# Performance work log

Hardware: AMD Instinct MI355X
Metric: run time of the kernel (lower is better)

## Reference

```python
import jax, jax.numpy as jnp
import numpy as np

T, B = 384, 128
IN_DIM, HID, OUT_DIM = 512, 1024, 512


def _lstm_step(h, c, x_t, Wx, Wh, b):
    # x_t: [B, D], h/c: [B, H]; gates order: i, f, g, o
    gates = x_t @ Wx + h @ Wh + b  # [B, 4H]
    i, f, g, o = jnp.split(gates, 4, axis=-1)
    c_new = jax.nn.sigmoid(f) * c + jax.nn.sigmoid(i) * jnp.tanh(g)
    h_new = jax.nn.sigmoid(o) * jnp.tanh(c_new)
    return h_new, c_new


def setup_inputs() -> dict:
    key = jax.random.key(0)
    ks = jax.random.split(key, 9)
    s_in = 1.0 / np.sqrt(IN_DIM)
    s_h = 1.0 / np.sqrt(HID)
    s_o = 1.0 / np.sqrt(OUT_DIM)
    return {
        "x": jax.random.normal(ks[0], (T, B, IN_DIM), dtype=jnp.float32),
        "hidden_state": jnp.zeros((1, B, HID), dtype=jnp.float32),
        "cell_state": jnp.zeros((1, B, HID), dtype=jnp.float32),
        "enc_Wx": jax.random.normal(ks[1], (IN_DIM, 4 * HID), dtype=jnp.float32) * s_in,
        "enc_Wh": jax.random.normal(ks[2], (HID, 4 * HID), dtype=jnp.float32) * s_h,
        "enc_b": jnp.zeros((4 * HID,), dtype=jnp.float32),
        "dec_Wx": jax.random.normal(ks[3], (OUT_DIM, 4 * HID), dtype=jnp.float32) * s_o,
        "dec_Wh": jax.random.normal(ks[4], (HID, 4 * HID), dtype=jnp.float32) * s_h,
        "dec_b": jnp.zeros((4 * HID,), dtype=jnp.float32),
        "fc_W": jax.random.normal(ks[5], (HID, OUT_DIM), dtype=jnp.float32) * s_h,
        "fc_b": jnp.zeros((OUT_DIM,), dtype=jnp.float32),
    }


def reference(x, hidden_state, cell_state, enc_Wx, enc_Wh, enc_b,
              dec_Wx, dec_Wh, dec_b, fc_W, fc_b):
    # ---- encoder: run LSTM over T steps, keep only final hidden state ----
    h0, c0 = hidden_state[0], cell_state[0]  # [B, H]

    def enc_step(carry, x_t):
        h, c = carry
        h, c = _lstm_step(h, c, x_t, enc_Wx, enc_Wh, enc_b)
        return (h, c), None

    (h_enc, _), _ = jax.lax.scan(enc_step, (h0, c0), x)

    y0 = jnp.zeros((B, OUT_DIM), dtype=x.dtype)
    c_dec0 = jnp.zeros((B, HID), dtype=x.dtype)

    def dec_step(carry, _):
        y, h, c = carry
        h, c = _lstm_step(h, c, y, dec_Wx, dec_Wh, dec_b)
        y = jax.nn.softmax(h @ fc_W + fc_b, axis=-1)  # softmax over dim=2
        return (y, h, c), y

    _, output = jax.lax.scan(dec_step, (y0, h_enc, c_dec0), None, length=T)
    return output  # [T, B, OUT_DIM]
```

## Files before the change

kernel.cpp:

```cpp
#include <hip/hip_runtime.h>


#define TS 384

typedef __attribute__((ext_vector_type(8))) short bf16x8;
typedef __attribute__((ext_vector_type(4))) float f32x4;

#define WS_XR 4096u
#define XR_SLOT 262144u
#define WS_HP (WS_XR + 4u*XR_SLOT)
#define HP_BUF 524288u
#define WS_FPN (WS_HP + 2u*HP_BUF)
#define WS_TOTAL (WS_FPN + 2097152u)

#define MFMA __builtin_amdgcn_mfma_f32_16x16x32_bf16

__device__ __forceinline__ unsigned short bf16r(float v) {
  unsigned u = __float_as_uint(v);
  u += 0x7FFFu + ((u >> 16) & 1u);
  return (unsigned short)(u >> 16);
}
__device__ __forceinline__ float bf2f(unsigned short h) {
  return __uint_as_float(((unsigned)h) << 16);
}
__device__ __forceinline__ void split2(float v, short& hi, short& lo) {
  unsigned short h = bf16r(v);
  float r = v - bf2f(h);
  hi = (short)h; lo = (short)bf16r(r);
}
__device__ __forceinline__ float sigm(float v)  { return 1.0f / (1.0f + __expf(-v)); }
__device__ __forceinline__ float tanhfa(float v){ return 1.0f - 2.0f / (__expf(2.0f*v) + 1.0f); }

__device__ __forceinline__ void st_u64(void* p, unsigned long long v) {
  __hip_atomic_store((unsigned long long*)p, v, __ATOMIC_RELAXED, __HIP_MEMORY_SCOPE_AGENT);
}
__device__ __forceinline__ unsigned long long ld_u64(const void* p) {
  return __hip_atomic_load((const unsigned long long*)p, __ATOMIC_RELAXED, __HIP_MEMORY_SCOPE_AGENT);
}
__device__ __forceinline__ void st_u32(unsigned* p, unsigned v) {
  __hip_atomic_store(p, v, __ATOMIC_RELAXED, __HIP_MEMORY_SCOPE_AGENT);
}
__device__ __forceinline__ void st_f32(float* p, float v) {
  __hip_atomic_store(p, v, __ATOMIC_RELAXED, __HIP_MEMORY_SCOPE_AGENT);
}
__device__ __forceinline__ float ld_f32(const float* p) {
  return __hip_atomic_load(p, __ATOMIC_RELAXED, __HIP_MEMORY_SCOPE_AGENT);
}
union FRAG { unsigned long long q[2]; bf16x8 v; };
__device__ __forceinline__ bf16x8 ld_frag(const short* base) {
  FRAG u;
  u.q[0] = ld_u64(base);
  u.q[1] = ld_u64(base + 4);
  return u.v;
}

__device__ __forceinline__ void setflag(unsigned* flag, unsigned val) {
  asm volatile("s_waitcnt vmcnt(0)" ::: "memory");
  __syncthreads();
  if (threadIdx.x == 0)
    __hip_atomic_store(flag, val, __ATOMIC_RELAXED, __HIP_MEMORY_SCOPE_AGENT);
}
__device__ __forceinline__ void wait_hier(const unsigned* flags, unsigned* pub,
    int aggIdx, int nPub, unsigned target, bool fence, int* sDead) {
  const int t = threadIdx.x;
  if (aggIdx >= 0) {
    if (t < 8) {
      const unsigned long long* q = (const unsigned long long*)(flags + aggIdx * 32 + t * 4);
      unsigned spins = 0;
      for (;;) {
        unsigned long long q0 = ld_u64(q), q1 = ld_u64(q + 1);
        bool ok = ((unsigned)q0 >= target) && ((unsigned)(q0 >> 32) >= target)
               && ((unsigned)q1 >= target) && ((unsigned)(q1 >> 32) >= target);
        if (__all(ok)) break;
        __builtin_amdgcn_s_sleep(1);
        if (++spins > (1u << 19)) { if (t == 0) *sDead = 1; break; }
      }
    }
    if (t == 0) st_u32(&pub[aggIdx], target);
  }
  if (t == 0) {
    unsigned spins = 0;
    for (;;) {
      bool ok = true;
      #pragma unroll
      for (int i = 0; i < 4; ++i) {
        if (i * 2 < nPub) {
          unsigned long long q0 = ld_u64((const unsigned long long*)pub + i);
          if (!((unsigned)q0 >= target && (unsigned)(q0 >> 32) >= target)) ok = false;
        }
      }
      if (ok) break;
      __builtin_amdgcn_s_sleep(1);
      if (++spins > (1u << 19)) { *sDead = 1; break; }
    }
    if (fence) __builtin_amdgcn_fence(__ATOMIC_ACQUIRE, "agent");
  }
  __syncthreads();
}
__device__ __forceinline__ void wait64(const unsigned* flags, unsigned target, int* sDead) {
  if (threadIdx.x < 16) {
    const unsigned long long* q = (const unsigned long long*)(flags + threadIdx.x * 4);
    unsigned spins = 0;
    for (;;) {
      unsigned long long q0 = ld_u64(q), q1 = ld_u64(q + 1);
      bool ok = ((unsigned)q0 >= target) && ((unsigned)(q0 >> 32) >= target)
             && ((unsigned)q1 >= target) && ((unsigned)(q1 >> 32) >= target);
      if (__all(ok)) break;
      __builtin_amdgcn_s_sleep(1);
      if (++spins > (1u << 19)) { if (threadIdx.x == 0) *sDead = 1; break; }
    }
  }
  __syncthreads();
}

__device__ void load_gate_weights(const float* __restrict__ Wx, const float* __restrict__ Wh,
                                  int p, short* sBh, short* sBl) {
  for (int idx = threadIdx.x; idx < 24576; idx += 1024) {
    int j = idx & 7, l = (idx >> 3) & 63, kb = idx >> 9;
    int k = kb * 32 + ((l >> 4) << 3) + j;
    int c = l & 15;
    int gcol = (c >> 2) * 1024 + p * 4 + (c & 3);
    float wv = (k < 512) ? Wx[(size_t)k * 4096 + gcol]
                         : Wh[(size_t)(k - 512) * 4096 + gcol];
    short hi, lo; split2(wv, hi, lo);
    sBh[idx] = hi; sBl[idx] = lo;
  }
}
__device__ void load_fc_weights(const float* __restrict__ fcW, int kg, int cg,
                                short* sFh, short* sFl) {
  for (int idx = threadIdx.x; idx < 4096; idx += 1024) {
    int j = idx & 7, l = (idx >> 3) & 63, kb = idx >> 9;
    int unit = kg * 256 + kb * 32 + ((l >> 4) << 3) + j;
    int col = cg * 16 + (l & 15);
    short hi, lo; split2(fcW[(size_t)unit * 512 + col], hi, lo);
    sFh[idx] = hi; sFl[idx] = lo;
  }
}

template<int NKB, int D>
__device__ __forceinline__ void gg_pipe(const short* AH_, const short* AL_,
    const short* BH_, const short* BL_, int mt, int l,
    int kbA0, int kbB0, f32x4* acc)
{
  const bf16x8* AH = (const bf16x8*)AH_;
  const bf16x8* AL = (const bf16x8*)AL_;
  const bf16x8* BH = (const bf16x8*)BH_;
  const bf16x8* BL = (const bf16x8*)BL_;
  bf16x8 pah[D], pal[D];
  #pragma unroll
  for (int i = 0; i < D; ++i) {
    pah[i] = AH[((kbA0 + i) * 8 + mt) * 64 + l];
    pal[i] = AL[((kbA0 + i) * 8 + mt) * 64 + l];
  }
  #pragma unroll
  for (int i = 0; i < NKB; ++i) {
    bf16x8 ah = pah[i % D], al = pal[i % D];
    if (i + D < NKB) {
      pah[i % D] = AH[((kbA0 + i + D) * 8 + mt) * 64 + l];
      pal[i % D] = AL[((kbA0 + i + D) * 8 + mt) * 64 + l];
    }
    bf16x8 bh = BH[(kbB0 + i) * 64 + l];
    bf16x8 bl = BL[(kbB0 + i) * 64 + l];
    const int a = (i & 1) * 3;
    acc[a + 0] = MFMA(ah, bh, acc[a + 0], 0, 0, 0);
    acc[a + 1] = MFMA(ah, bl, acc[a + 1], 0, 0, 0);
    acc[a + 2] = MFMA(al, bh, acc[a + 2], 0, 0, 0);
  }
}
__device__ __forceinline__ void gg_finish(f32x4* acc, int kh, int mt, int l,
                                          float* LDSgate) {
  f32x4 s = (acc[0] + acc[3]) + ((acc[1] + acc[4]) + (acc[2] + acc[5]));
  const int col = l & 15, r0 = mt * 16 + ((l >> 4) << 2);
  float* plane = LDSgate + kh * 2176;
  #pragma unroll
  for (int j = 0; j < 4; ++j) plane[(r0 + j) * 17 + col] = s[j];
}

__device__ __forceinline__ void conv_x(const float* __restrict__ xsrc,
                                       short* dstH, short* dstL, int p, int tl) {
  if (tl < 32) {
    int g = p * 32 + tl;
    int l = g & 63, mt = (g >> 6) & 7, kb = g >> 9;
    int row = mt * 16 + (l & 15), k = kb * 32 + ((l >> 4) << 3);
    const float* xs = xsrc + (size_t)row * 512 + k;
    unsigned long long h64[2] = {0, 0}, l64[2] = {0, 0};
    #pragma unroll
    for (int j = 0; j < 8; ++j) {
      short hi, lo; split2(xs[j], hi, lo);
      h64[j >> 2] |= (unsigned long long)(unsigned short)hi << ((j & 3) * 16);
      l64[j >> 2] |= (unsigned long long)(unsigned short)lo << ((j & 3) * 16);
    }
    int off = g * 8;
    st_u64(dstH + off, h64[0]); st_u64(dstH + off + 4, h64[1]);
    st_u64(dstL + off, l64[0]); st_u64(dstL + off + 4, l64[1]);
  }
}

__global__ void __launch_bounds__(1024, 1)
lstm9(const float* __restrict__ x, const float* __restrict__ h0p,
      const float* __restrict__ c0p, const float* __restrict__ eWx,
      const float* __restrict__ eWh, const float* __restrict__ eb,
      const float* __restrict__ dWx, const float* __restrict__ dWh,
      const float* __restrict__ db, const float* __restrict__ fcW,
      const float* __restrict__ fcb, float* __restrict__ out,
      char* __restrict__ ws)
{
  __shared__ __align__(16) short sBh[24576], sBl[24576];
  __shared__ __align__(16) short sFh[4096], sFl[4096];
  __shared__ float LDSgate[2 * 2176];
  __shared__ unsigned hsplit[512];
  __shared__ float ybuf[512];
  __shared__ float red[16];
  __shared__ int sDead;

  const int p = blockIdx.x, t = threadIdx.x;
  const int w = t >> 6, l = t & 63;
  const int mt = w & 7, kh = w >> 3;
  if (t == 0) sDead = 0;

  unsigned* hflag = (unsigned*)ws;
  unsigned* yflag = (unsigned*)(ws + 1024);
  unsigned* fflag = (unsigned*)(ws + 2048);
  unsigned* hpub  = (unsigned*)(ws + 3072);
  unsigned* ypub  = (unsigned*)(ws + 3200);
  unsigned* fpub  = (unsigned*)(ws + 3328);

  const int hagg = (p < 8) ? p : -1;
  const int yagg = (p >= 8 && p < 12) ? p - 8 : -1;
  const int fagg = (p >= 12 && p < 16) ? p - 12 : -1;

  short* xrH[4]; short* xrL[4];
  #pragma unroll
  for (int s4 = 0; s4 < 4; ++s4) {
    xrH[s4] = (short*)(ws + WS_XR + s4 * XR_SLOT);
    xrL[s4] = (short*)(ws + WS_XR + s4 * XR_SLOT + 131072u);
  }
  short* hpH[2]; short* hpL[2];
  #pragma unroll
  for (int b2 = 0; b2 < 2; ++b2) {
    hpH[b2] = (short*)(ws + WS_HP + b2 * HP_BUF);
    hpL[b2] = (short*)(ws + WS_HP + b2 * HP_BUF + 262144u);
  }
  float* fp = (float*)(ws + WS_FPN);

  const int row_pw = t & 127, u_pw = (t >> 7) & 3;

  load_gate_weights(eWx, eWh, p, sBh, sBl);
  conv_x(x, xrH[0], xrL[0], p, t);
  conv_x(x + 65536, xrH[1], xrL[1], p, t);
  if (t < 64) {
    int hg = p * 64 + t;
    int ll = hg & 63, mtt = (hg >> 6) & 7, hk = hg >> 9;
    int row = mtt * 16 + (ll & 15), k = hk * 32 + ((ll >> 4) << 3);
    const float* hs = h0p + (size_t)row * 1024 + k;
    unsigned long long h64[2] = {0, 0}, l64[2] = {0, 0};
    #pragma unroll
    for (int j = 0; j < 8; ++j) {
      short hi, lo; split2(hs[j], hi, lo);
      h64[j >> 2] |= (unsigned long long)(unsigned short)hi << ((j & 3) * 16);
      l64[j >> 2] |= (unsigned long long)(unsigned short)lo << ((j & 3) * 16);
    }
    int off = hg * 8;
    st_u64(hpH[0] + off, h64[0]); st_u64(hpH[0] + off + 4, h64[1]);
    st_u64(hpL[0] + off, l64[0]); st_u64(hpL[0] + off + 4, l64[1]);
  }
  float creg = 0.f, bq0 = 0.f, bq1 = 0.f, bq2 = 0.f, bq3 = 0.f;
  if (t < 512) {
    creg = c0p[(size_t)row_pw * 1024 + p * 4 + u_pw];
    bq0 = eb[0 * 1024 + p * 4 + u_pw];
    bq1 = eb[1 * 1024 + p * 4 + u_pw];
    bq2 = eb[2 * 1024 + p * 4 + u_pw];
    bq3 = eb[3 * 1024 + p * 4 + u_pw];
  }
  setflag(&hflag[p], 1u);
  wait_hier(hflag, hpub, hagg, 8, 1u, true, &sDead);
  if (sDead) return;

  for (int st = 0; st < TS; ++st) {
    int rb = st & 1, wb = rb ^ 1, xs = st & 3;
    f32x4 z = {0.f, 0.f, 0.f, 0.f};
    f32x4 acc[6] = {z, z, z, z, z, z};
    gg_pipe<8, 4>(xrH[xs], xrL[xs], sBh, sBl, mt, l, kh * 8, kh * 8, acc);
    wait_hier(hflag, hpub, hagg, 8, (unsigned)(st + 1), true, &sDead);
    if (sDead) return;
    gg_pipe<16, 4>(hpH[rb], hpL[rb], sBh, sBl, mt, l, kh * 16, 16 + kh * 16, acc);
    gg_finish(acc, kh, mt, l, LDSgate);
    __syncthreads();
    if (t < 512) {
      float g0 = LDSgate[row_pw * 17 + 0  + u_pw] + LDSgate[2176 + row_pw * 17 + 0  + u_pw] + bq0;
      float g1 = LDSgate[row_pw * 17 + 4  + u_pw] + LDSgate[2176 + row_pw * 17 + 4  + u_pw] + bq1;
      float g2 = LDSgate[row_pw * 17 + 8  + u_pw] + LDSgate[2176 + row_pw * 17 + 8  + u_pw] + bq2;
      float g3 = LDSgate[row_pw * 17 + 12 + u_pw] + LDSgate[2176 + row_pw * 17 + 12 + u_pw] + bq3;
      creg = sigm(g1) * creg + sigm(g0) * tanhfa(g2);
      float h = sigm(g3) * tanhfa(creg);
      short hi, lo; split2(h, hi, lo);
      hsplit[u_pw * 128 + row_pw] = ((unsigned)(unsigned short)hi << 16) | (unsigned short)lo;
    } else if (st + 2 < TS) {
      conv_x(x + (size_t)(st + 2) * 65536, xrH[(st + 2) & 3], xrL[(st + 2) & 3], p, t - 512);
    }
    __syncthreads();
    if (t < 128) {
      int r = t;
      unsigned w0 = hsplit[r], w1 = hsplit[128 + r], w2 = hsplit[256 + r], w3 = hsplit[384 + r];
      unsigned long long hi64 = (unsigned long long)(w0 >> 16)
        | ((unsigned long long)(w1 >> 16) << 16)
        | ((unsigned long long)(w2 >> 16) << 32)
        | ((unsigned long long)(w3 >> 16) << 48);
      unsigned long long lo64 = (unsigned long long)(w0 & 0xFFFFu)
        | ((unsigned long long)(w1 & 0xFFFFu) << 16)
        | ((unsigned long long)(w2 & 0xFFFFu) << 32)
        | ((unsigned long long)(w3 & 0xFFFFu) << 48);
      int hk = p >> 3, mtt = r >> 4;
      int lane_ = (((p >> 1) & 3) << 4) | (r & 15);
      int off = ((hk * 8 + mtt) * 64 + lane_) * 8 + (p & 1) * 4;
      st_u64(hpH[wb] + off, hi64);
      st_u64(hpL[wb] + off, lo64);
    }
    setflag(&hflag[p], (unsigned)(st + 2));
  }

  load_gate_weights(dWx, dWh, p, sBh, sBl);
  if (p >= 128) load_fc_weights(fcW, (p - 128) >> 5, (p - 128) & 31, sFh, sFl);
  if (t < 32) {
    int off = (p * 32 + t) * 8;
    st_u64(xrH[0] + off, 0ull); st_u64(xrH[0] + off + 4, 0ull);
    st_u64(xrL[0] + off, 0ull); st_u64(xrL[0] + off + 4, 0ull);
  }
  creg = 0.0f;
  if (t < 512) {
    bq0 = db[0 * 1024 + p * 4 + u_pw];
    bq1 = db[1 * 1024 + p * 4 + u_pw];
    bq2 = db[2 * 1024 + p * 4 + u_pw];
    bq3 = db[3 * 1024 + p * 4 + u_pw];
  }
  float fcb_r = (t < 512) ? fcb[t] : 0.f;
  setflag(&hflag[p], (unsigned)(TS + 2));

  const unsigned DB = (unsigned)(TS + 2);
  for (int st = 0; st < TS; ++st) {
    int rb = st & 1, wb = rb ^ 1;
    int ys = st & 1, yw = ys ^ 1;
    f32x4 z = {0.f, 0.f, 0.f, 0.f};
    f32x4 acc[6] = {z, z, z, z, z, z};
    wait_hier(hflag, hpub, hagg, 8, DB + (unsigned)st, true, &sDead);
    if (sDead) return;
    gg_pipe<16, 4>(hpH[rb], hpL[rb], sBh, sBl, mt, l, kh * 16, 16 + kh * 16, acc);
    wait_hier(yflag, ypub, yagg, 4, (unsigned)st, false, &sDead);
    if (sDead) return;
    gg_pipe<8, 4>(xrH[ys], xrL[ys], sBh, sBl, mt, l, kh * 8, kh * 8, acc);
    gg_finish(acc, kh, mt, l, LDSgate);
    __syncthreads();
    if (t < 512) {
      float g0 = LDSgate[row_pw * 17 + 0  + u_pw] + LDSgate[2176 + row_pw * 17 + 0  + u_pw] + bq0;
      float g1 = LDSgate[row_pw * 17 + 4  + u_pw] + LDSgate[2176 + row_pw * 17 + 4  + u_pw] + bq1;
      float g2 = LDSgate[row_pw * 17 + 8  + u_pw] + LDSgate[2176 + row_pw * 17 + 8  + u_pw] + bq2;
      float g3 = LDSgate[row_pw * 17 + 12 + u_pw] + LDSgate[2176 + row_pw * 17 + 12 + u_pw] + bq3;
      creg = sigm(g1) * creg + sigm(g0) * tanhfa(g2);
      float h = sigm(g3) * tanhfa(creg);
      short hi, lo; split2(h, hi, lo);
      hsplit[u_pw * 128 + row_pw] = ((unsigned)(unsigned short)hi << 16) | (unsigned short)lo;
    }
    __syncthreads();
    if (t < 128) {
      int r = t;
      unsigned w0 = hsplit[r], w1 = hsplit[128 + r], w2 = hsplit[256 + r], w3 = hsplit[384 + r];
      unsigned long long hi64 = (unsigned long long)(w0 >> 16)
        | ((unsigned long long)(w1 >> 16) << 16)
        | ((unsigned long long)(w2 >> 16) << 32)
        | ((unsigned long long)(w3 >> 16) << 48);
      unsigned long long lo64 = (unsigned long long)(w0 & 0xFFFFu)
        | ((unsigned long long)(w1 & 0xFFFFu) << 16)
        | ((unsigned long long)(w2 & 0xFFFFu) << 32)
        | ((unsigned long long)(w3 & 0xFFFFu) << 48);
      int hk = p >> 3, mtt = r >> 4;
      int lane_ = (((p >> 1) & 3) << 4) | (r & 15);
      int off = ((hk * 8 + mtt) * 64 + lane_) * 8 + (p & 1) * 4;
      st_u64(hpH[wb] + off, hi64);
      st_u64(hpL[wb] + off, lo64);
    }
    setflag(&hflag[p], DB + (unsigned)(st + 1));

    if (p >= 128) {
      const int f = p - 128, kg = f >> 5, cg = f & 31;
      wait64(hflag + kg * 64, DB + (unsigned)(st + 1), &sDead);
      if (sDead) return;
      {
        const bf16x8* FB = (const bf16x8*)sFh;
        const bf16x8* FL = (const bf16x8*)sFl;
        bf16x8 fah[4], fal[4];
        #pragma unroll
        for (int kb = 0; kb < 4; ++kb) {
          int gkb = kg * 8 + kh * 4 + kb;
          fah[kb] = ld_frag(hpH[wb] + ((gkb * 8 + mt) * 64 + l) * 8);
          fal[kb] = ld_frag(hpL[wb] + ((gkb * 8 + mt) * 64 + l) * 8);
        }
        f32x4 a0 = z, a1 = z, a2 = z;
        #pragma unroll
        for (int kb = 0; kb < 4; ++kb) {
          bf16x8 bh = FB[(kh * 4 + kb) * 64 + l];
          bf16x8 bl = FL[(kh * 4 + kb) * 64 + l];
          a0 = MFMA(fah[kb], bh, a0, 0, 0, 0);
          a1 = MFMA(fah[kb], bl, a1, 0, 0, 0);
          a2 = MFMA(fal[kb], bh, a2, 0, 0, 0);
        }
        f32x4 s = a0 + (a1 + a2);
        int slice = kg * 2 + kh;
        int col = cg * 16 + (l & 15), r0 = mt * 16 + ((l >> 4) << 2);
        #pragma unroll
        for (int j = 0; j < 4; ++j)
          st_f32(&fp[(size_t)(slice * 128 + r0 + j) * 512 + col], s[j]);
      }
      setflag(&fflag[f], (unsigned)(st + 1));
    } else {
      wait_hier(fflag, fpub, fagg, 4, (unsigned)(st + 1), false, &sDead);
      if (sDead) return;
      float v = 0.f, e = 0.f, mx;
      if (t < 512) {
        float tv[8];
        #pragma unroll
        for (int s8 = 0; s8 < 8; ++s8)
          tv[s8] = ld_f32(&fp[(size_t)(s8 * 128 + p) * 512 + t]);
        v = fcb_r + ((tv[0] + tv[1]) + (tv[2] + tv[3]))
                  + ((tv[4] + tv[5]) + (tv[6] + tv[7]));
        mx = v;
        #pragma unroll
        for (int o = 32; o > 0; o >>= 1) mx = fmaxf(mx, __shfl_xor(mx, o));
        if (l == 0) red[w] = mx;
      }
      __syncthreads();
      if (t < 512) {
        mx = red[0];
        #pragma unroll
        for (int i = 1; i < 8; ++i) mx = fmaxf(mx, red[i]);
        e = __expf(v - mx);
        float ss = e;
        #pragma unroll
        for (int o = 32; o > 0; o >>= 1) ss += __shfl_xor(ss, o);
        if (l == 0) red[8 + w] = ss;
      }
      __syncthreads();
      if (t < 512) {
        float ss = (red[8] + red[9]) + (red[10] + red[11])
                 + (red[12] + red[13]) + (red[14] + red[15]);
        float y = e / ss;
        out[((size_t)st * 128 + p) * 512 + t] = y;
        ybuf[t] = y;
      }
      __syncthreads();
      if (t < 64) {
        int kb = t >> 2, seg = t & 3;
        int k = kb * 32 + seg * 8;
        int lane_ = (seg << 4) | (p & 15), mtt = p >> 4;
        int off = ((kb * 8 + mtt) * 64 + lane_) * 8;
        unsigned long long h64[2] = {0, 0}, l64[2] = {0, 0};
        #pragma unroll
        for (int j = 0; j < 8; ++j) {
          short hi, lo; split2(ybuf[k + j], hi, lo);
          h64[j >> 2] |= (unsigned long long)(unsigned short)hi << ((j & 3) * 16);
          l64[j >> 2] |= (unsigned long long)(unsigned short)lo << ((j & 3) * 16);
        }
        st_u64(xrH[yw] + off, h64[0]); st_u64(xrH[yw] + off + 4, h64[1]);
        st_u64(xrL[yw] + off, l64[0]); st_u64(xrL[yw] + off + 4, l64[1]);
      }
      setflag(&yflag[p], (unsigned)(st + 1));
    }
  }
}

extern "C" void kernel_launch(void* const* d_in, const int* in_sizes, int n_in,
                              void* d_out, int out_size, void* d_ws, size_t ws_size,
                              hipStream_t stream) {
  const float* x   = (const float*)d_in[0];
  const float* h0  = (const float*)d_in[1];
  const float* c0  = (const float*)d_in[2];
  const float* eWx = (const float*)d_in[3];
  const float* eWh = (const float*)d_in[4];
  const float* eb  = (const float*)d_in[5];
  const float* dWx = (const float*)d_in[6];
  const float* dWh = (const float*)d_in[7];
  const float* db  = (const float*)d_in[8];
  const float* fcW = (const float*)d_in[9];
  const float* fcb = (const float*)d_in[10];
  float* out = (float*)d_out;

  if (ws_size < (size_t)WS_TOTAL) {
    hipMemsetAsync(d_out, 0xFF, (size_t)out_size * sizeof(float), stream);
    return;
  }
  hipMemsetAsync(d_ws, 0, 4096, stream);
  hipLaunchKernelGGL(lstm9, dim3(256), dim3(1024), 0, stream,
                     x, h0, c0, eWx, eWh, eb, dWx, dWh, db, fcW, fcb, out,
                     (char*)d_ws);
}
```

Baseline: 16.65 ms.

## Elect per-XCD leader for h-barrier and invalidate L2 only via leader handoff

Replaces the two-level hierarchical h-flag barrier (8 aggregator blocks plus publish flags, each block doing an acquire fence) with a per-XCD scheme. The first block on each XCD is elected leader: it polls all 256 flags, does the acquire fence and publishes a per-XCD done line. The other blocks on that XCD spin on that line and issue a lighter buffer_inv. This is meant to cut barrier latency and redundant cache invalidations per step, but relies on the XCC_ID hardware register and on cache-coherence assumptions about sc0 invalidation within an XCD. Output stores also become relaxed atomic stores.

```diff
diff --git a/kernel.cpp b/kernel.cpp
--- a/kernel.cpp
+++ b/kernel.cpp
@@ -40,6 +40,9 @@
 __device__ __forceinline__ void st_u32(unsigned* p, unsigned v) {
   __hip_atomic_store(p, v, __ATOMIC_RELAXED, __HIP_MEMORY_SCOPE_AGENT);
 }
+__device__ __forceinline__ unsigned ld_u32(const unsigned* p) {
+  return __hip_atomic_load(p, __ATOMIC_RELAXED, __HIP_MEMORY_SCOPE_AGENT);
+}
 __device__ __forceinline__ void st_f32(float* p, float v) {
   __hip_atomic_store(p, v, __ATOMIC_RELAXED, __HIP_MEMORY_SCOPE_AGENT);
 }
@@ -60,8 +63,41 @@
   if (threadIdx.x == 0)
     __hip_atomic_store(flag, val, __ATOMIC_RELAXED, __HIP_MEMORY_SCOPE_AGENT);
 }
+__device__ __forceinline__ void hwait(const unsigned* flags, unsigned* invdone_line,
+                                      bool leader, unsigned target, int* sDead) {
+  if (leader) {
+    if (threadIdx.x < 64) {
+      const unsigned long long* q = (const unsigned long long*)(flags + threadIdx.x * 4);
+      unsigned spins = 0;
+      for (;;) {
+        unsigned long long q0 = ld_u64(q), q1 = ld_u64(q + 1);
+        bool ok = ((unsigned)q0 >= target) && ((unsigned)(q0 >> 32) >= target)
+               && ((unsigned)q1 >= target) && ((unsigned)(q1 >> 32) >= target);
+        if (__all(ok)) break;
+        __builtin_amdgcn_s_sleep(1);
+        if (++spins > (1u << 19)) { if (threadIdx.x == 0) *sDead = 1; break; }
+      }
+    }
+    if (threadIdx.x == 0) {
+      __builtin_amdgcn_fence(__ATOMIC_ACQUIRE, "agent");
+      st_u32(invdone_line, target);
+      asm volatile("s_waitcnt vmcnt(0)" ::: "memory");
+    }
+  } else {
+    if (threadIdx.x == 0) {
+      unsigned spins = 0;
+      while (ld_u32(invdone_line) < target) {
+        __builtin_amdgcn_s_sleep(1);
+        if (++spins > (1u << 19)) { *sDead = 1; break; }
+      }
+      asm volatile("buffer_inv sc0" ::: "memory");
+      asm volatile("s_waitcnt vmcnt(0)" ::: "memory");
+    }
+  }
+  __syncthreads();
+}
 __device__ __forceinline__ void wait_hier(const unsigned* flags, unsigned* pub,
-    int aggIdx, int nPub, unsigned target, bool fence, int* sDead) {
+    int aggIdx, int nPub, unsigned target, int* sDead) {
   const int t = threadIdx.x;
   if (aggIdx >= 0) {
     if (t < 8) {
@@ -93,7 +129,6 @@
       __builtin_amdgcn_s_sleep(1);
       if (++spins > (1u << 19)) { *sDead = 1; break; }
     }
-    if (fence) __builtin_amdgcn_fence(__ATOMIC_ACQUIRE, "agent");
   }
   __syncthreads();
 }
@@ -197,13 +232,13 @@
 }
 
 __global__ void __launch_bounds__(1024, 1)
-lstm9(const float* __restrict__ x, const float* __restrict__ h0p,
-      const float* __restrict__ c0p, const float* __restrict__ eWx,
-      const float* __restrict__ eWh, const float* __restrict__ eb,
-      const float* __restrict__ dWx, const float* __restrict__ dWh,
-      const float* __restrict__ db, const float* __restrict__ fcW,
-      const float* __restrict__ fcb, float* __restrict__ out,
-      char* __restrict__ ws)
+lstm11(const float* __restrict__ x, const float* __restrict__ h0p,
+       const float* __restrict__ c0p, const float* __restrict__ eWx,
+       const float* __restrict__ eWh, const float* __restrict__ eb,
+       const float* __restrict__ dWx, const float* __restrict__ dWh,
+       const float* __restrict__ db, const float* __restrict__ fcW,
+       const float* __restrict__ fcb, float* __restrict__ out,
+       char* __restrict__ ws)
 {
   __shared__ __align__(16) short sBh[24576], sBl[24576];
   __shared__ __align__(16) short sFh[4096], sFl[4096];
@@ -211,7 +246,7 @@
   __shared__ unsigned hsplit[512];
   __shared__ float ybuf[512];
   __shared__ float red[16];
-  __shared__ int sDead;
+  __shared__ int sDead, sLeader, sXcd;
 
   const int p = blockIdx.x, t = threadIdx.x;
   const int w = t >> 6, l = t & 63;
@@ -221,11 +256,23 @@
   unsigned* hflag = (unsigned*)ws;
   unsigned* yflag = (unsigned*)(ws + 1024);
   unsigned* fflag = (unsigned*)(ws + 2048);
-  unsigned* hpub  = (unsigned*)(ws + 3072);
-  unsigned* ypub  = (unsigned*)(ws + 3200);
-  unsigned* fpub  = (unsigned*)(ws + 3328);
-
-  const int hagg = (p < 8) ? p : -1;
+  unsigned* ypub  = (unsigned*)(ws + 3072);
+  unsigned* fpub  = (unsigned*)(ws + 3136);
+  unsigned* elect = (unsigned*)(ws + 3264);
+
+  if (t == 0) {
+    unsigned xcd;
+    asm volatile("s_getreg_b32 %0, hwreg(HW_REG_XCC_ID)" : "=s"(xcd));
+    xcd &= 7u;
+    sXcd = (int)xcd;
+    unsigned old = __hip_atomic_fetch_add(&elect[xcd], 1u, __ATOMIC_ACQ_REL,
+                                          __HIP_MEMORY_SCOPE_AGENT);
+    sLeader = (old == 0u) ? 1 : 0;
+  }
+  __syncthreads();
+  const bool leader = (sLeader != 0);
+  unsigned* invd = (unsigned*)(ws + 3328 + sXcd * 64);
+
   const int yagg = (p >= 8 && p < 12) ? p - 8 : -1;
   const int fagg = (p >= 12 && p < 16) ? p - 12 : -1;
 
@@ -273,7 +320,7 @@
     bq3 = eb[3 * 1024 + p * 4 + u_pw];
   }
   setflag(&hflag[p], 1u);
-  wait_hier(hflag, hpub, hagg, 8, 1u, true, &sDead);
+  hwait(hflag, invd, leader, 1u, &sDead);
   if (sDead) return;
 
   for (int st = 0; st < TS; ++st) {
@@ -281,7 +328,7 @@
     f32x4 z = {0.f, 0.f, 0.f, 0.f};
     f32x4 acc[6] = {z, z, z, z, z, z};
     gg_pipe<8, 4>(xrH[xs], xrL[xs], sBh, sBl, mt, l, kh * 8, kh * 8, acc);
-    wait_hier(hflag, hpub, hagg, 8, (unsigned)(st + 1), true, &sDead);
+    hwait(hflag, invd, leader, (unsigned)(st + 1), &sDead);
     if (sDead) return;
     gg_pipe<16, 4>(hpH[rb], hpL[rb], sBh, sBl, mt, l, kh * 16, 16 + kh * 16, acc);
     gg_finish(acc, kh, mt, l, LDSgate);
@@ -342,10 +389,10 @@
     int ys = st & 1, yw = ys ^ 1;
     f32x4 z = {0.f, 0.f, 0.f, 0.f};
     f32x4 acc[6] = {z, z, z, z, z, z};
-    wait_hier(hflag, hpub, hagg, 8, DB + (unsigned)st, true, &sDead);
+    hwait(hflag, invd, leader, DB + (unsigned)st, &sDead);
     if (sDead) return;
     gg_pipe<16, 4>(hpH[rb], hpL[rb], sBh, sBl, mt, l, kh * 16, 16 + kh * 16, acc);
-    wait_hier(yflag, ypub, yagg, 4, (unsigned)st, false, &sDead);
+    wait_hier(yflag, ypub, yagg, 4, (unsigned)st, &sDead);
     if (sDead) return;
     gg_pipe<8, 4>(xrH[ys], xrL[ys], sBh, sBl, mt, l, kh * 8, kh * 8, acc);
     gg_finish(acc, kh, mt, l, LDSgate);
@@ -412,7 +459,7 @@
       }
       setflag(&fflag[f], (unsigned)(st + 1));
     } else {
-      wait_hier(fflag, fpub, fagg, 4, (unsigned)(st + 1), false, &sDead);
+      wait_hier(fflag, fpub, fagg, 4, (unsigned)(st + 1), &sDead);
       if (sDead) return;
       float v = 0.f, e = 0.f, mx;
       if (t < 512) {
@@ -443,7 +490,7 @@
         float ss = (red[8] + red[9]) + (red[10] + red[11])
                  + (red[12] + red[13]) + (red[14] + red[15]);
         float y = e / ss;
-        out[((size_t)st * 128 + p) * 512 + t] = y;
+        st_f32(&out[((size_t)st * 128 + p) * 512 + t], y);
         ybuf[t] = y;
       }
       __syncthreads();
@@ -488,7 +535,7 @@
     return;
   }
   hipMemsetAsync(d_ws, 0, 4096, stream);
-  hipLaunchKernelGGL(lstm9, dim3(256), dim3(1024), 0, stream,
+  hipLaunchKernelGGL(lstm11, dim3(256), dim3(1024), 0, stream,
                      x, h0, c0, eWx, eWh, eb, dWx, dWh, db, fcW, fcb, out,
                      (char*)d_ws);
 }
```

Result: faster. 15.13 ms (-9.2%).
